# Kernel optimization log

Hardware: AMD Instinct MI355X
Metric: run time of the kernel (lower is better)

Reference implementation:

```python
import jax, jax.numpy as jnp
import numpy as np

N = 4096; B = 4; NPB = N // B; K = 16
C = 128; COUT = 128; LMAX = 2; L = (LMAX + 1) ** 2  # 9 SH coefficients
H = 8; A = 8; V = 16; HV = H * V
F = 256; NB = 128; FD = 256; CUTOFF = 3.0
E = N * K

def _silu(x):
    return x * jax.nn.sigmoid(x)

def _mish(x):
    return x * jnp.tanh(jax.nn.softplus(x))

def _rms_norm(x, gamma):
    # degree-wise RMS over channel dim, x: [N, L, C]
    s = jnp.sqrt(jnp.mean(x * x, axis=-1, keepdims=True) + 1e-6)
    return x / s * gamma

def _rot_l1(x, R):
    # rotate the l=1 block (coeffs 1:4) of x [E, L, C] by R [E, 3, 3]
    l1 = jnp.einsum('eij,ejc->eic', R, x[:, 1:4, :])
    return jnp.concatenate([x[:, :1, :], l1, x[:, 4:, :]], axis=1)

def _knn(coord, batch):
    d2 = jnp.sum((coord[:, None, :] - coord[None, :, :]) ** 2, axis=-1)  # [N,N]
    same = batch[:, None] == batch[None, :]
    big = jnp.asarray(1e9, d2.dtype)
    d2 = jnp.where(same, d2, big)
    d2 = d2.at[jnp.arange(N), jnp.arange(N)].set(big)
    neg, idx = jax.lax.top_k(-d2, K)
    dist = jnp.sqrt(jnp.maximum(-neg, 0.0))
    edge_src = idx.reshape(-1)                       # [E]
    edge_dst = jnp.repeat(jnp.arange(N), K)          # [E]
    valid = (dist <= CUTOFF).reshape(-1)
    return edge_src, edge_dst, valid

def _edge_rot_mat(edge_vec):
    # deterministic rotation aligning each edge with the y-axis (eSCN-style)
    nx = edge_vec / (jnp.linalg.norm(edge_vec, axis=-1, keepdims=True) + 1e-12)
    ref = jnp.where(jnp.abs(nx[:, :1]) < 0.9,
                    jnp.array([1.0, 0.0, 0.0], nx.dtype),
                    jnp.array([0.0, 1.0, 0.0], nx.dtype))
    nz = jnp.cross(nx, ref)
    nz = nz / (jnp.linalg.norm(nz, axis=-1, keepdims=True) + 1e-12)
    ny = jnp.cross(nz, nx)
    return jnp.stack([nz, nx, ny], axis=1)  # [E,3,3]; R @ edge_dir = e_y

def _forward(node_coord, node_emb, batch, condition,
             W_e1, b_e1, W_e2, b_e2, W_src, W_dst, w_a, W_v, W_o,
             gamma1, gamma2, W_g, W_f1, W_f2, W_film, b_film):
    # dynamic KNN graph; geometry detached as in original (edge_vec.detach())
    coord_g = jax.lax.stop_gradient(node_coord)
    edge_src, edge_dst, valid = _knn(coord_g, batch)
    edge_vec = coord_g[edge_src] - coord_g[edge_dst]                  # [E,3]
    edge_len = jnp.linalg.norm(edge_vec, axis=-1)                     # [E]
    R = _edge_rot_mat(edge_vec)                                       # [E,3,3]
    # gaussian radial basis -> per-edge embedding
    mu = jnp.linspace(0.0, CUTOFF, NB)
    sigma = CUTOFF / NB
    rbf = jnp.exp(-0.5 * ((edge_len[:, None] - mu) / sigma) ** 2)     # [E,NB]
    edge_h = _silu(rbf @ W_e1 + b_e1) @ W_e2 + b_e2                   # [E,HV]
    # equivariant attention (rotate into edge frame, attend, rotate back)
    x_src = _rot_l1(node_emb[edge_src], R)                            # [E,L,C]
    q = node_emb[edge_dst, 0] @ W_dst + x_src[:, 0] @ W_src           # [E,H*A]
    logits = jnp.einsum('eha,ha->eh', _silu(q).reshape(E, H, A), w_a)
    logits = jnp.where(valid[:, None], logits, -1e9)
    m = jax.ops.segment_max(logits, edge_dst, num_segments=N)
    ex = jnp.exp(logits - m[edge_dst])
    den = jax.ops.segment_sum(ex, edge_dst, num_segments=N)
    attn = ex / (den[edge_dst] + 1e-9)                                # [E,H]
    v = jnp.einsum('elc,cv->elv', x_src, W_v) * edge_h[:, None, :]    # [E,L,HV]
    v = v.reshape(E, L, H, V) * attn[:, None, :, None]
    msg = _rot_l1(v.reshape(E, L, HV), jnp.swapaxes(R, 1, 2))         # back to global frame
    agg = jax.ops.segment_sum(msg, edge_dst, num_segments=N)          # [N,L,HV]
    x = node_emb + jnp.einsum('nlv,vc->nlc', agg, W_o)
    # FFN with separable S2 (scalar-gated) activation
    h = _rms_norm(x, gamma2)
    gate = _silu(h[:, 0] @ W_g)                                       # [N,F]
    hid = jnp.einsum('nlc,cf->nlf', h, W_f1) * gate[:, None, :]
    x = x + jnp.einsum('nlf,fo->nlo', hid, W_f2)
    x = _rms_norm(x, gamma1)
    # FiLM conditioning over flattened (L*C) per batch element
    film = _mish(condition) @ W_film + b_film                         # [B, 2*L*COUT]
    w, bfi = film[:, :L * COUT], film[:, L * COUT:]
    c = x.reshape(B, NPB, L * COUT) * w[:, None, :] + bfi[:, None, :]
    return c.reshape(N, L, COUT)

def setup_inputs():
    key = jax.random.key(0)
    ks = jax.random.split(key, 16)
    node_coord = jax.random.uniform(ks[0], (N, 3)) * 2.0
    node_emb = jax.random.normal(ks[1], (N, L, C)) * 0.1
    batch = jnp.arange(N, dtype=jnp.int64 if jax.config.jax_enable_x64 else jnp.int32) // NPB
    condition = jax.random.normal(ks[2], (B, FD))
    s = lambda d: 1.0 / np.sqrt(d)
    return {
        'node_coord': node_coord, 'node_emb': node_emb, 'batch': batch, 'condition': condition,
        'W_e1': jax.random.normal(ks[3], (NB, 128)) * s(NB), 'b_e1': jnp.zeros((128,)),
        'W_e2': jax.random.normal(ks[4], (128, HV)) * s(128), 'b_e2': jnp.zeros((HV,)),
        'W_src': jax.random.normal(ks[5], (C, H * A)) * s(C),
        'W_dst': jax.random.normal(ks[6], (C, H * A)) * s(C),
        'w_a': jax.random.normal(ks[7], (H, A)) * s(A),
        'W_v': jax.random.normal(ks[8], (C, HV)) * s(C),
        'W_o': jax.random.normal(ks[9], (HV, C)) * s(HV),
        'gamma1': jnp.ones((C,)), 'gamma2': jnp.ones((C,)),
        'W_g': jax.random.normal(ks[10], (C, F)) * s(C),
        'W_f1': jax.random.normal(ks[11], (C, F)) * s(C),
        'W_f2': jax.random.normal(ks[12], (F, COUT)) * s(F),
        'W_film': jax.random.normal(ks[13], (FD, 2 * L * COUT)) * s(FD),
        'b_film': jnp.zeros((2 * L * COUT,)),
    }

def reference(node_coord, node_emb, batch, condition,
              W_e1, b_e1, W_e2, b_e2, W_src, W_dst, w_a, W_v, W_o,
              gamma1, gamma2, W_g, W_f1, W_f2, W_film, b_film):
    out = _forward(node_coord, node_emb, batch, condition,
                   W_e1, b_e1, W_e2, b_e2, W_src, W_dst, w_a, W_v, W_o,
                   gamma1, gamma2, W_g, W_f1, W_f2, W_film, b_film)
    return (node_coord, out, batch)
```

## Files before the change

### kernel.cpp

```cpp
#include <hip/hip_runtime.h>

#define NNODE 4096
#define NPB   1024

__device__ __forceinline__ float siluf(float x){ return x / (1.0f + expf(-x)); }

__global__ __launch_bounds__(256) void k_film(const float* __restrict__ cond,
                                              const float* __restrict__ Wfilm,
                                              const float* __restrict__ bfilm,
                                              float* __restrict__ filmG){
  __shared__ float mL[256];
  int b = blockIdx.y;
  int t = threadIdx.x;
  int j = blockIdx.x*256 + t;
  float x = cond[b*256 + t];
  float sp = fmaxf(x, 0.f) + log1pf(expf(-fabsf(x)));
  mL[t] = x * tanhf(sp);
  __syncthreads();
  if(j >= 2304) return;
  float acc = bfilm[j];
  for(int i=0;i<256;i++) acc += mL[i] * Wfilm[i*2304 + j];
  filmG[b*2304 + j] = acc;
}

__global__ __launch_bounds__(128) void k_pre(const float* __restrict__ emb,
                                             const float* __restrict__ Wv,
                                             const float* __restrict__ Wsrc,
                                             const float* __restrict__ Wdst,
                                             float* __restrict__ ZG,
                                             float* __restrict__ QsG,
                                             float* __restrict__ QdG){
  __shared__ __align__(16) float Es[1152];
  const int n = blockIdx.x;
  const int t = threadIdx.x;
  {
    const float4* src = (const float4*)(emb + (size_t)n*1152);
    float4* dst = (float4*)Es;
    for(int idx=t; idx<288; idx+=128) dst[idx] = src[idx];
  }
  __syncthreads();
  float z[9];
  #pragma unroll
  for(int l=0;l<9;l++) z[l]=0.f;
  for(int c4=0;c4<32;c4++){
    float w0 = Wv[(c4*4+0)*128 + t];
    float w1 = Wv[(c4*4+1)*128 + t];
    float w2 = Wv[(c4*4+2)*128 + t];
    float w3 = Wv[(c4*4+3)*128 + t];
    #pragma unroll
    for(int l=0;l<9;l++){
      float4 x4 = *(const float4*)&Es[l*128 + c4*4];
      z[l] += x4.x*w0 + x4.y*w1 + x4.z*w2 + x4.w*w3;
    }
  }
  #pragma unroll
  for(int l=0;l<9;l++) ZG[(size_t)n*1152 + l*128 + t] = z[l];
  {
    const float* W = (t < 64) ? Wsrc : Wdst;
    const int col = t & 63;
    float q = 0.f;
    for(int c=0;c<128;c++) q += Es[c] * W[c*64 + col];
    if(t < 64) QsG[n*64 + col] = q;
    else       QdG[n*64 + col] = q;
  }
}

#define E_HD   0
#define E_QS   0
#define E_QD   1024
#define E_LG   1088
#define E_SX   1216
#define E_EH   2048
#define E_RBW  4096
#define E_AT   4352
#define E_KI   4480
#define E_KD   4496
#define E_LEN  4512
#define E_VL   4528
#define E_W0   4544
#define E_NPF  4608
__global__ __launch_bounds__(256) void k_edge(
    const float* __restrict__ coord,
    const float* __restrict__ We1, const float* __restrict__ be1,
    const float* __restrict__ We2, const float* __restrict__ be2,
    const float* __restrict__ wa,
    const float* __restrict__ Qs, const float* __restrict__ Qd,
    const float* __restrict__ Z,
    float* __restrict__ out){
  __shared__ __align__(16) float S[2*E_NPF];
  int* Si = (int*)S;
  const int t = threadIdx.x;
  const int h = t >> 7;
  const int u = t & 127;
  const int n = blockIdx.x*2 + h;
  const int base = n & ~(NPB - 1);
  const int self = n - base;
  const int NP = h * E_NPF;
  float* aggG = out + 12288;

  for(int idx = t; idx < 3072; idx += 256) S[idx] = coord[base*3 + idx];
  __syncthreads();
  const float cx = S[self*3+0];
  const float cy = S[self*3+1];
  const float cz = S[self*3+2];
  if((t & 64) == 0){
    int lane = t & 63;
    float d2a[16]; int ida[16];
    for(int q=0;q<16;q++){
      int j = lane + q*64;
      float dx = __fsub_rn(S[j*3+0], cx);
      float dy = __fsub_rn(S[j*3+1], cy);
      float dz = __fsub_rn(S[j*3+2], cz);
      float d2 = __fadd_rn(__fadd_rn(__fmul_rn(dx,dx), __fmul_rn(dy,dy)), __fmul_rn(dz,dz));
      if(j == self) d2 = 3e38f;
      d2a[q] = d2; ida[q] = j;
    }
    for(int r=0;r<16;r++){
      float bd = d2a[0]; int bi = ida[0];
      for(int q=1;q<16;q++){
        bool bet = (d2a[q] < bd) || (d2a[q] == bd && ida[q] < bi);
        if(bet){ bd = d2a[q]; bi = ida[q]; }
      }
      for(int s=1;s<64;s<<=1){
        float od = __shfl_xor(bd, s, 64);
        int   oi = __shfl_xor(bi, s, 64);
        bool bet = (od < bd) || (od == bd && oi < bi);
        if(bet){ bd = od; bi = oi; }
      }
      if(lane == 0){ Si[NP + E_KI + r] = bi; S[NP + E_KD + r] = bd; }
      for(int q=0;q<16;q++) if(ida[q] == bi) d2a[q] = 3e38f;
    }
  }
  __syncthreads();

  if(u < 16){
    float len = __fsqrt_rn(S[NP + E_KD + u]);
    S[NP + E_LEN + u] = len;
    S[NP + E_VL + u]  = (len <= 3.0f) ? 1.0f : 0.0f;
    int i0 = (int)(len * (127.0f/3.0f) + 0.5f);
    int w0 = i0 - 7;
    w0 = w0 < 0 ? 0 : (w0 > 112 ? 112 : w0);
    Si[NP + E_W0 + u] = w0;
  }
  for(int idx = u; idx < 1024; idx += 128){
    int e = idx >> 6, ha = idx & 63;
    int src = base + Si[NP + E_KI + e];
    S[NP + E_QS + idx] = Qs[src*64 + ha];
  }
  if(u < 64) S[NP + E_QD + u] = Qd[n*64 + u];
  __syncthreads();

  {
    int e = u >> 3, hh = u & 7;
    float s = 0.f;
    #pragma unroll
    for(int a=0;a<8;a++){
      float q = S[NP + E_QD + hh*8 + a] + S[NP + E_QS + e*64 + hh*8 + a];
      s += siluf(q) * wa[hh*8 + a];
    }
    S[NP + E_LG + u] = (S[NP + E_VL + e] > 0.5f) ? s : -1e9f;

    const float step = 3.0f/127.0f;
    const float sigma = 3.0f/128.0f;
    for(int idx = u; idx < 256; idx += 128){
      int e2 = idx >> 4, w = idx & 15;
      int bin = Si[NP + E_W0 + e2] + w;
      float d = (S[NP + E_LEN + e2] - step*(float)bin) / sigma;
      S[NP + E_RBW + idx] = expf(-0.5f*d*d);
    }
  }
  __syncthreads();

  if(u < 8){
    float m = -3e38f;
    for(int r=0;r<16;r++) m = fmaxf(m, S[NP + E_LG + r*8 + u]);
    S[NP + E_SX + u] = m;
  }
  __syncthreads();
  {
    float ex = expf(S[NP + E_LG + u] - S[NP + E_SX + (u & 7)]);
    __syncthreads();
    S[NP + E_LG + u] = ex;
    __syncthreads();
    if(u < 8){
      float d = 0.f;
      for(int r=0;r<16;r++) d += S[NP + E_LG + r*8 + u];
      S[NP + E_SX + 8 + u] = d;
    }
    __syncthreads();
    S[NP + E_AT + u] = ex / (S[NP + E_SX + 8 + (u & 7)] + 1e-9f);
  }
  __syncthreads();

  {
    float acc16[16];
    int   b0[16];
    #pragma unroll
    for(int e=0;e<16;e++){ acc16[e] = 0.f; b0[e] = Si[NP + E_W0 + e]; }
    for(int w=0; w<16; w++){
      #pragma unroll
      for(int e=0;e<16;e++){
        float rb = S[NP + E_RBW + e*16 + w];
        acc16[e] = fmaf(rb, We1[(b0[e] + w)*128 + u], acc16[e]);
      }
    }
    float b = be1[u];
    #pragma unroll
    for(int e=0;e<16;e++) S[NP + E_HD + e*128 + u] = siluf(acc16[e] + b);
  }
  __syncthreads();

  {
    float acc16[16];
    #pragma unroll
    for(int e=0;e<16;e++) acc16[e] = 0.f;
    for(int i4=0;i4<32;i4++){
      float w0 = We2[(i4*4+0)*128 + u];
      float w1 = We2[(i4*4+1)*128 + u];
      float w2 = We2[(i4*4+2)*128 + u];
      float w3 = We2[(i4*4+3)*128 + u];
      #pragma unroll
      for(int e=0;e<16;e++){
        float4 h4 = *(const float4*)&S[NP + E_HD + e*128 + i4*4];
        acc16[e] += h4.x*w0 + h4.y*w1 + h4.z*w2 + h4.w*w3;
      }
    }
    float b = be2[u];
    #pragma unroll
    for(int e=0;e<16;e++) S[NP + E_EH + e*128 + u] = acc16[e] + b;
  }
  __syncthreads();

  {
    float acc[9];
    #pragma unroll
    for(int l=0;l<9;l++) acc[l] = 0.f;
    #pragma unroll 4
    for(int e=0;e<16;e++){
      const float* zp = &Z[(size_t)(base + Si[NP + E_KI + e])*1152 + u];
      float sc = S[NP + E_EH + e*128 + u] * S[NP + E_AT + e*8 + (u>>4)];
      #pragma unroll
      for(int l=0;l<9;l++) acc[l] = fmaf(zp[l*128], sc, acc[l]);
    }
    #pragma unroll
    for(int l=0;l<9;l++) aggG[(size_t)n*1152 + l*128 + u] = acc[l];
  }
}

#define FF_AHL 0
#define FF_HID 4608
#define FF_RED 9216
#define FF_NLDS 9296
__global__ __launch_bounds__(256) void k_ffn(
    const float* __restrict__ emb,
    const float* __restrict__ Wo,
    const float* __restrict__ g1, const float* __restrict__ g2,
    const float* __restrict__ Wg, const float* __restrict__ Wf1,
    const float* __restrict__ Wf2,
    const float* __restrict__ filmG,
    float* __restrict__ out){
  __shared__ __align__(16) float S[FF_NLDS];
  const int t = threadIdx.x;
  const int n0 = blockIdx.x * 4;
  float* aggG = out + 12288;

  {
    const float4* src = (const float4*)(aggG + (size_t)n0*1152);
    float4* dst = (float4*)&S[FF_AHL];
    for(int i=t;i<1152;i+=256) dst[i] = src[i];
  }
  __syncthreads();

  const int u = t & 127, g = t >> 7;
  float x[2][9];
  #pragma unroll
  for(int j=0;j<2;j++)
    #pragma unroll
    for(int l=0;l<9;l++) x[j][l]=0.f;

  for(int c4=0;c4<32;c4++){
    float w0 = Wo[(c4*4+0)*128+u];
    float w1 = Wo[(c4*4+1)*128+u];
    float w2 = Wo[(c4*4+2)*128+u];
    float w3 = Wo[(c4*4+3)*128+u];
    #pragma unroll
    for(int j=0;j<2;j++)
      #pragma unroll
      for(int l=0;l<9;l++){
        float4 a4 = *(const float4*)&S[FF_AHL + ((2*g+j)*9+l)*128 + c4*4];
        x[j][l] += a4.x*w0 + a4.y*w1 + a4.z*w2 + a4.w*w3;
      }
  }

  #pragma unroll
  for(int j=0;j<2;j++)
    #pragma unroll
    for(int l=0;l<9;l++){
      x[j][l] += emb[(size_t)(n0+2*g+j)*1152 + l*128 + u];
      float sq = x[j][l]*x[j][l];
      #pragma unroll
      for(int s=1;s<64;s<<=1) sq += __shfl_xor(sq, s, 64);
      if((u&63)==0) S[FF_RED + ((2*g+j)*9+l)*2 + (u>>6)] = sq;
    }
  __syncthreads();

  {
    float g2u = g2[u];
    #pragma unroll
    for(int j=0;j<2;j++)
      #pragma unroll
      for(int l=0;l<9;l++){
        int r = (2*g+j)*9+l;
        float s = S[FF_RED + r*2] + S[FF_RED + r*2+1];
        float ss = sqrtf(s/128.f + 1e-6f);
        S[FF_AHL + r*128 + u] = x[j][l]/ss*g2u;
      }
  }
  __syncthreads();

  const int fc = t & 63, rg = t >> 6;
  for(int ft=0; ft<4; ft++){
    const int f0 = ft*64;
    float ha[9]; float gacc = 0.f;
    #pragma unroll
    for(int l=0;l<9;l++) ha[l]=0.f;
    for(int c4=0;c4<32;c4++){
      float wg0=Wg[(c4*4+0)*256+f0+fc], wg1=Wg[(c4*4+1)*256+f0+fc],
            wg2=Wg[(c4*4+2)*256+f0+fc], wg3=Wg[(c4*4+3)*256+f0+fc];
      float wa0=Wf1[(c4*4+0)*256+f0+fc], wa1=Wf1[(c4*4+1)*256+f0+fc],
            wa2=Wf1[(c4*4+2)*256+f0+fc], wa3=Wf1[(c4*4+3)*256+f0+fc];
      float4 h0 = *(const float4*)&S[FF_AHL + (rg*9+0)*128 + c4*4];
      gacc  += h0.x*wg0 + h0.y*wg1 + h0.z*wg2 + h0.w*wg3;
      ha[0] += h0.x*wa0 + h0.y*wa1 + h0.z*wa2 + h0.w*wa3;
      #pragma unroll
      for(int l=1;l<9;l++){
        float4 h4 = *(const float4*)&S[FF_AHL + (rg*9+l)*128 + c4*4];
        ha[l] += h4.x*wa0 + h4.y*wa1 + h4.z*wa2 + h4.w*wa3;
      }
    }
    {
      float gate = siluf(gacc);
      float* hb = &S[FF_HID + (ft&1)*2304];
      #pragma unroll
      for(int l=0;l<9;l++) hb[(rg*9+l)*64 + fc] = ha[l]*gate;
    }
    __syncthreads();
    const float* hbr = &S[FF_HID + (ft&1)*2304];
    for(int f4=0; f4<16; f4++){
      float w0 = Wf2[(f0+f4*4+0)*128 + u];
      float w1 = Wf2[(f0+f4*4+1)*128 + u];
      float w2 = Wf2[(f0+f4*4+2)*128 + u];
      float w3 = Wf2[(f0+f4*4+3)*128 + u];
      #pragma unroll
      for(int j=0;j<2;j++)
        #pragma unroll
        for(int l=0;l<9;l++){
          float4 h4 = *(const float4*)&hbr[((2*g+j)*9+l)*64 + f4*4];
          x[j][l] += h4.x*w0 + h4.y*w1 + h4.z*w2 + h4.w*w3;
        }
    }
  }

  #pragma unroll
  for(int j=0;j<2;j++)
    #pragma unroll
    for(int l=0;l<9;l++){
      float sq = x[j][l]*x[j][l];
      #pragma unroll
      for(int s=1;s<64;s<<=1) sq += __shfl_xor(sq, s, 64);
      if((u&63)==0) S[FF_RED + ((2*g+j)*9+l)*2 + (u>>6)] = sq;
    }
  __syncthreads();

  {
    float g1u = g1[u];
    int b = n0 >> 10;
    #pragma unroll
    for(int j=0;j<2;j++)
      #pragma unroll
      for(int l=0;l<9;l++){
        int r = (2*g+j)*9+l;
        float s = S[FF_RED + r*2] + S[FF_RED + r*2+1];
        float ss = sqrtf(s/128.f + 1e-6f);
        int jj = l*128 + u;
        float w  = filmG[b*2304 + jj];
        float bi = filmG[b*2304 + 1152 + jj];
        float y = x[j][l]/ss*g1u;
        out[12288 + (size_t)(n0+2*g+j)*1152 + jj] = y*w + bi;
      }
  }
}

__global__ __launch_bounds__(256) void k_copy(const float* __restrict__ coord,
                                              float* __restrict__ out){
  int i = blockIdx.x*256 + threadIdx.x;
  if(i < 12288) out[i] = coord[i];
  int n = i - 12288;
  if(n >= 0 && n < 4096) out[12288 + 4718592 + n] = (float)(n >> 10);
}

extern "C" void kernel_launch(void* const* d_in, const int* in_sizes, int n_in,
                              void* d_out, int out_size, void* d_ws, size_t ws_size,
                              hipStream_t stream) {
  const float* coord = (const float*)d_in[0];
  const float* emb   = (const float*)d_in[1];
  const float* cond  = (const float*)d_in[3];
  const float* We1   = (const float*)d_in[4];
  const float* be1   = (const float*)d_in[5];
  const float* We2   = (const float*)d_in[6];
  const float* be2   = (const float*)d_in[7];
  const float* Wsrc  = (const float*)d_in[8];
  const float* Wdst  = (const float*)d_in[9];
  const float* wa    = (const float*)d_in[10];
  const float* Wv    = (const float*)d_in[11];
  const float* Wo    = (const float*)d_in[12];
  const float* g1    = (const float*)d_in[13];
  const float* g2    = (const float*)d_in[14];
  const float* Wg    = (const float*)d_in[15];
  const float* Wf1   = (const float*)d_in[16];
  const float* Wf2   = (const float*)d_in[17];
  const float* Wfilm = (const float*)d_in[18];
  const float* bfilm = (const float*)d_in[19];

  float* outf  = (float*)d_out;
  float* filmG = (float*)d_ws;
  float* QsG   = filmG + 9216;
  float* QdG   = QsG + 262144;
  float* ZG    = QdG + 262144;

  k_film<<<dim3(9,4), 256, 0, stream>>>(cond, Wfilm, bfilm, filmG);
  k_pre<<<NNODE, 128, 0, stream>>>(emb, Wv, Wsrc, Wdst, ZG, QsG, QdG);
  k_edge<<<NNODE/2, 256, 0, stream>>>(coord, We1, be1, We2, be2, wa,
                                      QsG, QdG, ZG, outf);
  k_ffn<<<NNODE/4, 256, 0, stream>>>(emb, Wo, g1, g2, Wg, Wf1, Wf2,
                                     filmG, outf);
  k_copy<<<64, 256, 0, stream>>>(coord, outf);
}
```

Measured before the change: 446.8 us.

## Remap pre, edge and FFN kernels to wave-per-node with float2 channel pairs

The value projection now gives each thread two channels and about half the SH rows, using float2 weight loads; row 4 is computed by both halves. The edge kernel splits the 16 edges across two waves, each handling a channel pair, and drops the barrier between the two edge-MLP stages. The two waves' partial aggregations are combined through LDS with one barrier. The FFN kernel assigns one wave per node with private LDS slices, removing block-wide barriers and cross-wave reduction buffers and reading weights as float2. The trade-off is a higher register count per thread and reliance on wave-level lockstep for LDS reuse without barriers.

After: 442.6 us. Within noise of the previous version (-0.9%).

```diff
diff --git a/kernel.cpp b/kernel.cpp
--- a/kernel.cpp
+++ b/kernel.cpp
@@ -39,22 +39,28 @@
     for(int idx=t; idx<288; idx+=128) dst[idx] = src[idx];
   }
   __syncthreads();
-  float z[9];
-  #pragma unroll
-  for(int l=0;l<9;l++) z[l]=0.f;
+  const int l0 = (t>>6)*4;
+  const int c0 = (t&63)*2;
+  float z[5][2];
+  #pragma unroll
+  for(int il=0;il<5;il++){ z[il][0]=0.f; z[il][1]=0.f; }
   for(int c4=0;c4<32;c4++){
-    float w0 = Wv[(c4*4+0)*128 + t];
-    float w1 = Wv[(c4*4+1)*128 + t];
-    float w2 = Wv[(c4*4+2)*128 + t];
-    float w3 = Wv[(c4*4+3)*128 + t];
-    #pragma unroll
-    for(int l=0;l<9;l++){
-      float4 x4 = *(const float4*)&Es[l*128 + c4*4];
-      z[l] += x4.x*w0 + x4.y*w1 + x4.z*w2 + x4.w*w3;
-    }
-  }
-  #pragma unroll
-  for(int l=0;l<9;l++) ZG[(size_t)n*1152 + l*128 + t] = z[l];
+    float2 wv0 = *(const float2*)&Wv[(c4*4+0)*128 + c0];
+    float2 wv1 = *(const float2*)&Wv[(c4*4+1)*128 + c0];
+    float2 wv2 = *(const float2*)&Wv[(c4*4+2)*128 + c0];
+    float2 wv3 = *(const float2*)&Wv[(c4*4+3)*128 + c0];
+    #pragma unroll
+    for(int il=0;il<5;il++){
+      float4 x4 = *(const float4*)&Es[(l0+il)*128 + c4*4];
+      z[il][0] += x4.x*wv0.x + x4.y*wv1.x + x4.z*wv2.x + x4.w*wv3.x;
+      z[il][1] += x4.x*wv0.y + x4.y*wv1.y + x4.z*wv2.y + x4.w*wv3.y;
+    }
+  }
+  #pragma unroll
+  for(int il=0;il<5;il++){
+    float2 o; o.x = z[il][0]; o.y = z[il][1];
+    *(float2*)&ZG[(size_t)n*1152 + (l0+il)*128 + c0] = o;
+  }
   {
     const float* W = (t < 64) ? Wsrc : Wdst;
     const int col = t & 63;
@@ -192,65 +198,96 @@
   }
   __syncthreads();
 
-  {
-    float acc16[16];
-    int   b0[16];
-    #pragma unroll
-    for(int e=0;e<16;e++){ acc16[e] = 0.f; b0[e] = Si[NP + E_W0 + e]; }
-    for(int w=0; w<16; w++){
-      #pragma unroll
-      for(int e=0;e<16;e++){
-        float rb = S[NP + E_RBW + e*16 + w];
-        acc16[e] = fmaf(rb, We1[(b0[e] + w)*128 + u], acc16[e]);
-      }
-    }
-    float b = be1[u];
-    #pragma unroll
-    for(int e=0;e<16;e++) S[NP + E_HD + e*128 + u] = siluf(acc16[e] + b);
-  }
-  __syncthreads();
-
-  {
-    float acc16[16];
-    #pragma unroll
-    for(int e=0;e<16;e++) acc16[e] = 0.f;
-    for(int i4=0;i4<32;i4++){
-      float w0 = We2[(i4*4+0)*128 + u];
-      float w1 = We2[(i4*4+1)*128 + u];
-      float w2 = We2[(i4*4+2)*128 + u];
-      float w3 = We2[(i4*4+3)*128 + u];
-      #pragma unroll
-      for(int e=0;e<16;e++){
-        float4 h4 = *(const float4*)&S[NP + E_HD + e*128 + i4*4];
-        acc16[e] += h4.x*w0 + h4.y*w1 + h4.z*w2 + h4.w*w3;
-      }
-    }
-    float b = be2[u];
-    #pragma unroll
-    for(int e=0;e<16;e++) S[NP + E_EH + e*128 + u] = acc16[e] + b;
-  }
-  __syncthreads();
-
-  {
-    float acc[9];
-    #pragma unroll
-    for(int l=0;l<9;l++) acc[l] = 0.f;
-    #pragma unroll 4
-    for(int e=0;e<16;e++){
-      const float* zp = &Z[(size_t)(base + Si[NP + E_KI + e])*1152 + u];
-      float sc = S[NP + E_EH + e*128 + u] * S[NP + E_AT + e*8 + (u>>4)];
-      #pragma unroll
-      for(int l=0;l<9;l++) acc[l] = fmaf(zp[l*128], sc, acc[l]);
-    }
-    #pragma unroll
-    for(int l=0;l<9;l++) aggG[(size_t)n*1152 + l*128 + u] = acc[l];
-  }
-}
-
-#define FF_AHL 0
-#define FF_HID 4608
-#define FF_RED 9216
-#define FF_NLDS 9296
+  const int w2 = (t >> 6) & 1;
+  const int u2 = t & 63;
+  const int c0 = u2*2;
+  {
+    float a4[8][2]; int b0[8];
+    #pragma unroll
+    for(int k=0;k<8;k++){ a4[k][0]=0.f; a4[k][1]=0.f; b0[k] = Si[NP + E_W0 + 8*w2 + k]; }
+    for(int wi=0; wi<16; wi++){
+      #pragma unroll
+      for(int k=0;k<8;k++){
+        float rb = S[NP + E_RBW + (8*w2+k)*16 + wi];
+        float2 we = *(const float2*)&We1[(b0[k] + wi)*128 + c0];
+        a4[k][0] = fmaf(rb, we.x, a4[k][0]);
+        a4[k][1] = fmaf(rb, we.y, a4[k][1]);
+      }
+    }
+    float2 be = *(const float2*)&be1[c0];
+    #pragma unroll
+    for(int k=0;k<8;k++){
+      float2 o; o.x = siluf(a4[k][0] + be.x); o.y = siluf(a4[k][1] + be.y);
+      *(float2*)&S[NP + E_HD + (8*w2+k)*128 + c0] = o;
+    }
+  }
+
+  {
+    float a5[8][2];
+    #pragma unroll
+    for(int k=0;k<8;k++){ a5[k][0]=0.f; a5[k][1]=0.f; }
+    for(int c4=0;c4<32;c4++){
+      float2 w0 = *(const float2*)&We2[(c4*4+0)*128 + c0];
+      float2 w1 = *(const float2*)&We2[(c4*4+1)*128 + c0];
+      float2 w2v= *(const float2*)&We2[(c4*4+2)*128 + c0];
+      float2 w3 = *(const float2*)&We2[(c4*4+3)*128 + c0];
+      #pragma unroll
+      for(int k=0;k<8;k++){
+        float4 h4 = *(const float4*)&S[NP + E_HD + (8*w2+k)*128 + c4*4];
+        a5[k][0] += h4.x*w0.x + h4.y*w1.x + h4.z*w2v.x + h4.w*w3.x;
+        a5[k][1] += h4.x*w0.y + h4.y*w1.y + h4.z*w2v.y + h4.w*w3.y;
+      }
+    }
+    float2 be = *(const float2*)&be2[c0];
+    #pragma unroll
+    for(int k=0;k<8;k++){
+      float2 o; o.x = a5[k][0] + be.x; o.y = a5[k][1] + be.y;
+      *(float2*)&S[NP + E_EH + (8*w2+k)*128 + c0] = o;
+    }
+  }
+  __syncthreads();
+
+  {
+    float ag[9][2];
+    #pragma unroll
+    for(int l=0;l<9;l++){ ag[l][0]=0.f; ag[l][1]=0.f; }
+    #pragma unroll
+    for(int k=0;k<8;k++){
+      int e = 8*w2 + k;
+      const float* zp = &Z[(size_t)(base + Si[NP + E_KI + e])*1152 + c0];
+      float at = S[NP + E_AT + e*8 + (c0>>4)];
+      float2 eh2 = *(const float2*)&S[NP + E_EH + e*128 + c0];
+      float sc0 = eh2.x * at;
+      float sc1 = eh2.y * at;
+      #pragma unroll
+      for(int l=0;l<9;l++){
+        float2 z2 = *(const float2*)&zp[l*128];
+        ag[l][0] = fmaf(z2.x, sc0, ag[l][0]);
+        ag[l][1] = fmaf(z2.y, sc1, ag[l][1]);
+      }
+    }
+    if(w2 == 0){
+      #pragma unroll
+      for(int l=0;l<9;l++){
+        float2 o; o.x = ag[l][0]; o.y = ag[l][1];
+        *(float2*)&S[NP + l*128 + c0] = o;
+      }
+    }
+    __syncthreads();
+    if(w2 == 1){
+      #pragma unroll
+      for(int l=0;l<9;l++){
+        float2 p = *(const float2*)&S[NP + l*128 + c0];
+        float2 o; o.x = ag[l][0] + p.x; o.y = ag[l][1] + p.y;
+        *(float2*)&aggG[(size_t)n*1152 + l*128 + c0] = o;
+      }
+    }
+  }
+}
+
+#define FW_ACT 0
+#define FW_HID 1152
+#define FW_SZ  2304
 __global__ __launch_bounds__(256) void k_ffn(
     const float* __restrict__ emb,
     const float* __restrict__ Wo,
@@ -259,135 +296,123 @@
     const float* __restrict__ Wf2,
     const float* __restrict__ filmG,
     float* __restrict__ out){
-  __shared__ __align__(16) float S[FF_NLDS];
+  __shared__ __align__(16) float S[4*FW_SZ];
   const int t = threadIdx.x;
-  const int n0 = blockIdx.x * 4;
+  const int rg = t >> 6;
+  const int u2 = t & 63;
+  const int c0 = u2*2;
+  const int n = blockIdx.x*4 + rg;
+  float* W_ = &S[rg*FW_SZ];
   float* aggG = out + 12288;
 
   {
-    const float4* src = (const float4*)(aggG + (size_t)n0*1152);
-    float4* dst = (float4*)&S[FF_AHL];
-    for(int i=t;i<1152;i+=256) dst[i] = src[i];
-  }
-  __syncthreads();
-
-  const int u = t & 127, g = t >> 7;
-  float x[2][9];
-  #pragma unroll
-  for(int j=0;j<2;j++)
-    #pragma unroll
-    for(int l=0;l<9;l++) x[j][l]=0.f;
-
+    const float4* src = (const float4*)(aggG + (size_t)n*1152);
+    float4* dst = (float4*)&W_[FW_ACT];
+    for(int i=u2;i<288;i+=64) dst[i] = src[i];
+  }
+
+  float x[9][2];
+  #pragma unroll
+  for(int l=0;l<9;l++){ x[l][0]=0.f; x[l][1]=0.f; }
   for(int c4=0;c4<32;c4++){
-    float w0 = Wo[(c4*4+0)*128+u];
-    float w1 = Wo[(c4*4+1)*128+u];
-    float w2 = Wo[(c4*4+2)*128+u];
-    float w3 = Wo[(c4*4+3)*128+u];
-    #pragma unroll
-    for(int j=0;j<2;j++)
+    float2 w0 = *(const float2*)&Wo[(c4*4+0)*128 + c0];
+    float2 w1 = *(const float2*)&Wo[(c4*4+1)*128 + c0];
+    float2 w2 = *(const float2*)&Wo[(c4*4+2)*128 + c0];
+    float2 w3 = *(const float2*)&Wo[(c4*4+3)*128 + c0];
+    #pragma unroll
+    for(int l=0;l<9;l++){
+      float4 a4 = *(const float4*)&W_[FW_ACT + l*128 + c4*4];
+      x[l][0] += a4.x*w0.x + a4.y*w1.x + a4.z*w2.x + a4.w*w3.x;
+      x[l][1] += a4.x*w0.y + a4.y*w1.y + a4.z*w2.y + a4.w*w3.y;
+    }
+  }
+
+  float g2a = g2[c0], g2b = g2[c0+1];
+  #pragma unroll
+  for(int l=0;l<9;l++){
+    float2 e2 = *(const float2*)&emb[(size_t)n*1152 + l*128 + c0];
+    x[l][0] += e2.x; x[l][1] += e2.y;
+    float sq = x[l][0]*x[l][0] + x[l][1]*x[l][1];
+    #pragma unroll
+    for(int s=1;s<64;s<<=1) sq += __shfl_xor(sq, s, 64);
+    float ss = sqrtf(sq/128.f + 1e-6f);
+    float2 o; o.x = x[l][0]/ss*g2a; o.y = x[l][1]/ss*g2b;
+    *(float2*)&W_[FW_ACT + l*128 + c0] = o;
+  }
+
+  float ha[2][9][2]; float ga[2][2];
+  #pragma unroll
+  for(int ft=0;ft<2;ft++){
+    ga[ft][0]=0.f; ga[ft][1]=0.f;
+    #pragma unroll
+    for(int l=0;l<9;l++){ ha[ft][l][0]=0.f; ha[ft][l][1]=0.f; }
+  }
+  for(int c4=0;c4<32;c4++){
+    float2 wf[2][4], wg_[2][4];
+    #pragma unroll
+    for(int ft=0;ft<2;ft++)
+      #pragma unroll
+      for(int i=0;i<4;i++){
+        wf[ft][i]  = *(const float2*)&Wf1[(c4*4+i)*256 + ft*128 + c0];
+        wg_[ft][i] = *(const float2*)&Wg [(c4*4+i)*256 + ft*128 + c0];
+      }
+    float4 h0 = *(const float4*)&W_[FW_ACT + 0*128 + c4*4];
+    #pragma unroll
+    for(int ft=0;ft<2;ft++){
+      ga[ft][0] += h0.x*wg_[ft][0].x + h0.y*wg_[ft][1].x + h0.z*wg_[ft][2].x + h0.w*wg_[ft][3].x;
+      ga[ft][1] += h0.x*wg_[ft][0].y + h0.y*wg_[ft][1].y + h0.z*wg_[ft][2].y + h0.w*wg_[ft][3].y;
+      ha[ft][0][0] += h0.x*wf[ft][0].x + h0.y*wf[ft][1].x + h0.z*wf[ft][2].x + h0.w*wf[ft][3].x;
+      ha[ft][0][1] += h0.x*wf[ft][0].y + h0.y*wf[ft][1].y + h0.z*wf[ft][2].y + h0.w*wf[ft][3].y;
+    }
+    #pragma unroll
+    for(int l=1;l<9;l++){
+      float4 h4 = *(const float4*)&W_[FW_ACT + l*128 + c4*4];
+      #pragma unroll
+      for(int ft=0;ft<2;ft++){
+        ha[ft][l][0] += h4.x*wf[ft][0].x + h4.y*wf[ft][1].x + h4.z*wf[ft][2].x + h4.w*wf[ft][3].x;
+        ha[ft][l][1] += h4.x*wf[ft][0].y + h4.y*wf[ft][1].y + h4.z*wf[ft][2].y + h4.w*wf[ft][3].y;
+      }
+    }
+  }
+
+  #pragma unroll
+  for(int ft=0;ft<2;ft++){
+    float gx = siluf(ga[ft][0]), gy = siluf(ga[ft][1]);
+    #pragma unroll
+    for(int l=0;l<9;l++){
+      float2 o; o.x = ha[ft][l][0]*gx; o.y = ha[ft][l][1]*gy;
+      *(float2*)&W_[FW_HID + l*128 + c0] = o;
+    }
+    for(int f4=0;f4<32;f4++){
+      float2 w0 = *(const float2*)&Wf2[(ft*128 + f4*4+0)*128 + c0];
+      float2 w1 = *(const float2*)&Wf2[(ft*128 + f4*4+1)*128 + c0];
+      float2 w2 = *(const float2*)&Wf2[(ft*128 + f4*4+2)*128 + c0];
+      float2 w3 = *(const float2*)&Wf2[(ft*128 + f4*4+3)*128 + c0];
       #pragma unroll
       for(int l=0;l<9;l++){
-        float4 a4 = *(const float4*)&S[FF_AHL + ((2*g+j)*9+l)*128 + c4*4];
-        x[j][l] += a4.x*w0 + a4.y*w1 + a4.z*w2 + a4.w*w3;
-      }
-  }
-
-  #pragma unroll
-  for(int j=0;j<2;j++)
+        float4 h4 = *(const float4*)&W_[FW_HID + l*128 + f4*4];
+        x[l][0] += h4.x*w0.x + h4.y*w1.x + h4.z*w2.x + h4.w*w3.x;
+        x[l][1] += h4.x*w0.y + h4.y*w1.y + h4.z*w2.y + h4.w*w3.y;
+      }
+    }
+  }
+
+  {
+    float g1a = g1[c0], g1b = g1[c0+1];
+    int b = n >> 10;
     #pragma unroll
     for(int l=0;l<9;l++){
-      x[j][l] += emb[(size_t)(n0+2*g+j)*1152 + l*128 + u];
-      float sq = x[j][l]*x[j][l];
+      float sq = x[l][0]*x[l][0] + x[l][1]*x[l][1];
       #pragma unroll
       for(int s=1;s<64;s<<=1) sq += __shfl_xor(sq, s, 64);
-      if((u&63)==0) S[FF_RED + ((2*g+j)*9+l)*2 + (u>>6)] = sq;
-    }
-  __syncthreads();
-
-  {
-    float g2u = g2[u];
-    #pragma unroll
-    for(int j=0;j<2;j++)
-      #pragma unroll
-      for(int l=0;l<9;l++){
-        int r = (2*g+j)*9+l;
-        float s = S[FF_RED + r*2] + S[FF_RED + r*2+1];
-        float ss = sqrtf(s/128.f + 1e-6f);
-        S[FF_AHL + r*128 + u] = x[j][l]/ss*g2u;
-      }
-  }
-  __syncthreads();
-
-  const int fc = t & 63, rg = t >> 6;
-  for(int ft=0; ft<4; ft++){
-    const int f0 = ft*64;
-    float ha[9]; float gacc = 0.f;
-    #pragma unroll
-    for(int l=0;l<9;l++) ha[l]=0.f;
-    for(int c4=0;c4<32;c4++){
-      float wg0=Wg[(c4*4+0)*256+f0+fc], wg1=Wg[(c4*4+1)*256+f0+fc],
-            wg2=Wg[(c4*4+2)*256+f0+fc], wg3=Wg[(c4*4+3)*256+f0+fc];
-      float wa0=Wf1[(c4*4+0)*256+f0+fc], wa1=Wf1[(c4*4+1)*256+f0+fc],
-            wa2=Wf1[(c4*4+2)*256+f0+fc], wa3=Wf1[(c4*4+3)*256+f0+fc];
-      float4 h0 = *(const float4*)&S[FF_AHL + (rg*9+0)*128 + c4*4];
-      gacc  += h0.x*wg0 + h0.y*wg1 + h0.z*wg2 + h0.w*wg3;
-      ha[0] += h0.x*wa0 + h0.y*wa1 + h0.z*wa2 + h0.w*wa3;
-      #pragma unroll
-      for(int l=1;l<9;l++){
-        float4 h4 = *(const float4*)&S[FF_AHL + (rg*9+l)*128 + c4*4];
-        ha[l] += h4.x*wa0 + h4.y*wa1 + h4.z*wa2 + h4.w*wa3;
-      }
-    }
-    {
-      float gate = siluf(gacc);
-      float* hb = &S[FF_HID + (ft&1)*2304];
-      #pragma unroll
-      for(int l=0;l<9;l++) hb[(rg*9+l)*64 + fc] = ha[l]*gate;
-    }
-    __syncthreads();
-    const float* hbr = &S[FF_HID + (ft&1)*2304];
-    for(int f4=0; f4<16; f4++){
-      float w0 = Wf2[(f0+f4*4+0)*128 + u];
-      float w1 = Wf2[(f0+f4*4+1)*128 + u];
-      float w2 = Wf2[(f0+f4*4+2)*128 + u];
-      float w3 = Wf2[(f0+f4*4+3)*128 + u];
-      #pragma unroll
-      for(int j=0;j<2;j++)
-        #pragma unroll
-        for(int l=0;l<9;l++){
-          float4 h4 = *(const float4*)&hbr[((2*g+j)*9+l)*64 + f4*4];
-          x[j][l] += h4.x*w0 + h4.y*w1 + h4.z*w2 + h4.w*w3;
-        }
-    }
-  }
-
-  #pragma unroll
-  for(int j=0;j<2;j++)
-    #pragma unroll
-    for(int l=0;l<9;l++){
-      float sq = x[j][l]*x[j][l];
-      #pragma unroll
-      for(int s=1;s<64;s<<=1) sq += __shfl_xor(sq, s, 64);
-      if((u&63)==0) S[FF_RED + ((2*g+j)*9+l)*2 + (u>>6)] = sq;
-    }
-  __syncthreads();
-
-  {
-    float g1u = g1[u];
-    int b = n0 >> 10;
-    #pragma unroll
-    for(int j=0;j<2;j++)
-      #pragma unroll
-      for(int l=0;l<9;l++){
-        int r = (2*g+j)*9+l;
-        float s = S[FF_RED + r*2] + S[FF_RED + r*2+1];
-        float ss = sqrtf(s/128.f + 1e-6f);
-        int jj = l*128 + u;
-        float w  = filmG[b*2304 + jj];
-        float bi = filmG[b*2304 + 1152 + jj];
-        float y = x[j][l]/ss*g1u;
-        out[12288 + (size_t)(n0+2*g+j)*1152 + jj] = y*w + bi;
-      }
+      float ss = sqrtf(sq/128.f + 1e-6f);
+      float2 fw = *(const float2*)&filmG[b*2304 + l*128 + c0];
+      float2 fb = *(const float2*)&filmG[b*2304 + 1152 + l*128 + c0];
+      float2 o;
+      o.x = x[l][0]/ss*g1a*fw.x + fb.x;
+      o.y = x[l][1]/ss*g1b*fw.y + fb.y;
+      *(float2*)&out[12288 + (size_t)n*1152 + l*128 + c0] = o;
+    }
   }
 }
 
```
